# Performance work log

Hardware: AMD Instinct MI355X
Metric: run time of the kernel (lower is better)

## Reference

```python
import jax, jax.numpy as jnp
import numpy as np

N = 50000      # n_points (== n_support, non-strided)
H = 32         # neighbors per point
IN_F = 128
OUT_F = 256
MID = OUT_F // 4   # bottleneck width = 64
K = 15         # kernel points
RADIUS = 2.0
KP_EXTENT = 1.2 * RADIUS / 5.0  # config.KP_extent * radius / density_parameter
EPS = 1e-6
SLOPE = 0.1


def _wvar(k, size):
    # weight_variable: normal(scale=sqrt(2/size[-1])), zeroed outside 2*std
    std = np.sqrt(2.0 / size[-1])
    w = jax.random.normal(k, size, jnp.float32) * std
    return jnp.where(jnp.abs(w) > 2.0 * std, 0.0, w)


def setup_inputs():
    key = jax.random.key(0)
    ks = jax.random.split(key, 12)
    query_points = jax.random.uniform(ks[0], (N, 3), jnp.float32)
    support_points = query_points  # non-strided: same cloud
    neighbors_indices = jax.random.randint(ks[1], (N, H), 0, N, jnp.int32)
    features = jax.random.normal(ks[2], (N, IN_F), jnp.float32)
    kp = (jax.random.uniform(ks[3], (K, 3), jnp.float32) * 2.0 - 1.0) * (0.66 * KP_EXTENT)
    kernel_points = kp.at[0].set(0.0)  # fixed_kernel_points='center'
    w1 = _wvar(ks[4], (IN_F, MID))
    kw = _wvar(ks[5], (K, MID, MID))
    w3 = _wvar(ks[6], (MID, OUT_F))
    ws = _wvar(ks[7], (IN_F, OUT_F))
    def bnp(k, c):
        k1, k2 = jax.random.split(k)
        g = jax.random.uniform(k1, (c,), jnp.float32, 0.75, 1.25)
        b = jax.random.normal(k2, (c,), jnp.float32) * 0.1
        return g, b
    g1, b1 = bnp(ks[8], MID)
    g2, b2 = bnp(ks[9], MID)
    g3, b3 = bnp(ks[10], OUT_F)
    gs, bs = bnp(ks[11], OUT_F)
    return dict(query_points=query_points, support_points=support_points,
                neighbors_indices=neighbors_indices, features=features,
                kernel_points=kernel_points, w1=w1, g1=g1, b1=b1,
                kw=kw, g2=g2, b2=b2, w3=w3, g3=g3, b3=b3, ws=ws, gs=gs, bs=bs)


def _bn(x, g, b):
    # BatchNorm1d in training mode: batch statistics over points, biased var
    m = jnp.mean(x, 0)
    v = jnp.var(x, 0)
    return g * (x - m) * jax.lax.rsqrt(v + EPS) + b


def _lrelu(x):
    return jnp.where(x >= 0, x, SLOPE * x)


def _unary(x, w, g, b):
    return _lrelu(_bn(x @ w, g, b))


def _kpconv(q, s, inds, f, kp, kw):
    # pad support with a far shadow point and features with a zero row (faithful to KPConv)
    s_pad = jnp.concatenate([s, jnp.full((1, 3), 1e6, s.dtype)], 0)
    f_pad = jnp.concatenate([f, jnp.zeros((1, f.shape[1]), f.dtype)], 0)
    neigh = s_pad[inds]                        # [n,h,3] gather
    d = neigh - q[:, None, :]                  # [n,h,3]
    sq = jnp.sum((d[:, :, None, :] - kp[None, None, :, :]) ** 2, -1)  # [n,h,K]
    dist = jnp.sqrt(jnp.maximum(sq, 1e-12))
    infl = jnp.maximum(0.0, 1.0 - dist / KP_EXTENT)   # 'linear' KP_influence
    nf = f_pad[inds]                           # [n,h,d] gather
    wf = jnp.einsum('nhk,nhd->nkd', infl, nf)  # aggregate over neighbors
    return jnp.einsum('nkd,kdo->no', wf, kw)   # 'sum' aggregation over kernel pts


def reference(query_points, support_points, neighbors_indices, features, kernel_points,
              w1, g1, b1, kw, g2, b2, w3, g3, b3, ws, gs, bs):
    x = _unary(features, w1, g1, b1)                                     # conv1
    x = _lrelu(_bn(_kpconv(query_points, support_points, neighbors_indices,
                           x, kernel_points, kw), g2, b2))               # conv2 (KPConv)
    x = _unary(x, w3, g3, b3)                                            # conv3
    sc = _unary(features, ws, gs, bs)                                    # shortcut (non-strided)
    return _lrelu(sc + x)
```

## Files before the change

### kernel.cpp

```cpp
#include <hip/hip_runtime.h>

#define NPTS 50000
#define HN 32
#define INF1 128
#define OUTF3 256
#define MIDF 64
#define KP 15
#define EPSV 1e-6f
#define SLOPE 0.1f
#define KPE 0.48f
#define INVN (1.f / 50000.f)

typedef __attribute__((ext_vector_type(8))) short short8;
typedef __attribute__((ext_vector_type(4))) float float4v;
typedef unsigned short ushort;
typedef unsigned long long ull;

__device__ inline ushort f2bf(float f) {
    union { float f; unsigned u; } v; v.f = f;
    unsigned r = v.u + 0x7fff + ((v.u >> 16) & 1);
    return (ushort)(r >> 16);
}
__device__ inline float bf2f(ushort u) {
    union { unsigned u; float f; } v; v.u = ((unsigned)u) << 16;
    return v.f;
}


__global__ __launch_bounds__(256)
void k_repack_all(const float* __restrict__ w1, const float* __restrict__ wsw,
                  ushort* __restrict__ wpC,
                  const float* __restrict__ kw, ushort* __restrict__ wpk,
                  const float* __restrict__ w3, ushort* __restrict__ wp3) {
    int id = blockIdx.x * 256 + threadIdx.x;
    if (id < 5120) {
        int l = id & 63;
        int nt = (id >> 6) % 20, s = id / 1280;
        int n = nt * 16 + (l & 15);
        int k0 = s * 32 + ((l >> 4) & 3) * 8;
#pragma unroll
        for (int j = 0; j < 8; j++) {
            float v = (n < 64) ? w1[(k0 + j) * 64 + n] : wsw[(k0 + j) * 256 + (n - 64)];
            wpC[id * 8 + j] = f2bf(v);
        }
    } else if (id < 13312) {
        int id2 = id - 5120;
        int l2 = id2 & 63;
        int nt = (id2 >> 6) & 3, s = id2 >> 8;
        int n = nt * 16 + (l2 & 15);
        int kd0 = s * 32 + ((l2 >> 4) & 3) * 8;
#pragma unroll
        for (int j = 0; j < 8; j++) {
            int kd = kd0 + j, d = kd >> 4, kk = kd & 15;
            float v = (kk < KP) ? kw[kk * 4096 + d * 64 + n] : 0.f;
            wpk[id2 * 8 + j] = f2bf(v);
        }
    } else if (id < 15360) {
        int id3 = id - 13312;
        int l3 = id3 & 63;
        int nt = (id3 >> 6) % 16, s = id3 / 1024;
        int n = nt * 16 + (l3 & 15);
        int k0 = s * 32 + ((l3 >> 4) & 3) * 8;
#pragma unroll
        for (int j = 0; j < 8; j++)
            wp3[id3 * 8 + j] = f2bf(w3[(k0 + j) * 256 + n]);
    }
}

__global__ __launch_bounds__(256)
void k_conv1sc(const float* __restrict__ feat, const ushort* __restrict__ WpC,
               ushort* __restrict__ x1raw, ushort* __restrict__ scb,
               float* __restrict__ Sa1, float* __restrict__ Sq1,
               float* __restrict__ SaS, float* __restrict__ SqS, int M) {
    __shared__ float sred[320], qred[320];
    int t = threadIdx.x;
    int w = t >> 6, l = t & 63;
    int dl = l & 15, q4 = l >> 4;

    for (int c = t; c < 320; c += 256) { sred[c] = 0.f; qred[c] = 0.f; }
    __syncthreads();

    int m0 = blockIdx.x * 64 + w * 16;
    int row = m0 + dl;
    long arow = (row < M) ? row : (M - 1);
    const float* ap0 = feat + arow * INF1 + q4 * 8;
    short8 afr[4];
#pragma unroll
    for (int s = 0; s < 4; s++) {
        float4 a0 = *(const float4*)(ap0 + s * 32);
        float4 a1 = *(const float4*)(ap0 + s * 32 + 4);
        union { short8 v; ushort u[8]; } au;
        au.u[0] = f2bf(a0.x); au.u[1] = f2bf(a0.y); au.u[2] = f2bf(a0.z); au.u[3] = f2bf(a0.w);
        au.u[4] = f2bf(a1.x); au.u[5] = f2bf(a1.y); au.u[6] = f2bf(a1.z); au.u[7] = f2bf(a1.w);
        afr[s] = au.v;
    }
    const short8* Bp = (const short8*)WpC + l;
    int rb = q4 * 4;
#pragma unroll
    for (int half = 0; half < 2; half++) {
        float4v acc[10];
#pragma unroll
        for (int j = 0; j < 10; j++) acc[j] = (float4v){0.f, 0.f, 0.f, 0.f};
#pragma unroll
        for (int s = 0; s < 4; s++)
#pragma unroll
            for (int j = 0; j < 10; j++) {
                short8 bf = Bp[(s * 20 + half * 10 + j) * 64];
                acc[j] = __builtin_amdgcn_mfma_f32_16x16x32_bf16(afr[s], bf, acc[j], 0, 0, 0);
            }
#pragma unroll
        for (int r = 0; r < 4; r++) {
            int rr = m0 + rb + r;
            if (rr < M) {
                if (half == 0) {
                    ull pk = 0;
#pragma unroll
                    for (int j = 0; j < 4; j++)
                        pk |= ((ull)f2bf(acc[j][r])) << (16 * j);
                    *(ull*)(x1raw + (long)rr * 64 + 4 * dl) = pk;
#pragma unroll
                    for (int j = 4; j < 10; j++)
                        scb[(long)rr * 256 + (j * 16 + dl - 64)] = f2bf(acc[j][r]);
                } else {
#pragma unroll
                    for (int j = 0; j < 10; j++)
                        scb[(long)rr * 256 + ((10 + j) * 16 + dl - 64)] = f2bf(acc[j][r]);
                }
            }
        }
#pragma unroll
        for (int j = 0; j < 10; j++) {
            float s = 0.f, q = 0.f;
#pragma unroll
            for (int r = 0; r < 4; r++) {
                float v = ((m0 + rb + r) < M) ? acc[j][r] : 0.f;
                s += v; q += v * v;
            }
            s += __shfl_xor(s, 16); s += __shfl_xor(s, 32);
            q += __shfl_xor(q, 16); q += __shfl_xor(q, 32);
            if (q4 == 0) {
                atomicAdd(&sred[(half * 10 + j) * 16 + dl], s);
                atomicAdd(&qred[(half * 10 + j) * 16 + dl], q);
            }
        }
    }
    __syncthreads();
    for (int c = t; c < 320; c += 256) {
        if (c < 64) { atomicAdd(&Sa1[c], sred[c]); atomicAdd(&Sq1[c], qred[c]); }
        else        { atomicAdd(&SaS[c - 64], sred[c]); atomicAdd(&SqS[c - 64], qred[c]); }
    }
}

__global__ __launch_bounds__(256)
void k_bnx(const ushort* __restrict__ X, ushort* __restrict__ Y,
           const float* __restrict__ Sa, const float* __restrict__ Sq,
           const float* __restrict__ g, const float* __restrict__ b) {
    __shared__ float sc[64], sh[64];
    int t = threadIdx.x;
    if (t < 64) {
        float m = Sa[t] * INVN;
        float v = Sq[t] * INVN - m * m;
        float s = g[t] * rsqrtf(v + EPSV);
        sc[t] = s; sh[t] = b[t] - s * m;
    }
    __syncthreads();
    int i = blockIdx.x * 256 + t;
    long base = (long)i * 4;
    int dlp = i & 15;
    ull vin = *(const ull*)(X + base);
    ull vout = 0;
#pragma unroll
    for (int j = 0; j < 4; j++) {
        int c = j * 16 + dlp;
        float f = bf2f((ushort)((vin >> (16 * j)) & 0xffff));
        float v = f * sc[c] + sh[c];
        v = (v >= 0.f) ? v : SLOPE * v;
        vout |= ((ull)f2bf(v)) << (16 * j);
    }
    *(ull*)(Y + base) = vout;
}

__global__ __launch_bounds__(256)
void k_kpconv(const float* __restrict__ qpts, const float* __restrict__ spts,
              const int* __restrict__ nbr, const ushort* __restrict__ x1b,
              const float* __restrict__ kpp, const ushort* __restrict__ kwp,
              ushort* __restrict__ y, float* __restrict__ Sa, float* __restrict__ Sq) {
    __shared__ __align__(16) ushort wfs[16][1032];
    __shared__ float posd[4][3][HN];
    __shared__ int   sidx[4][HN];

    int t = threadIdx.x;
    int w = t >> 6, l = t & 63;
    int dl = l & 15, q4 = l >> 4;

    int kmin = (dl < KP) ? dl : (KP - 1);
    float kx = kpp[kmin * 3 + 0], ky = kpp[kmin * 3 + 1], kz = kpp[kmin * 3 + 2];

    for (int pp = 0; pp < 4; pp++) {
        int p = w * 4 + pp;
        int n = blockIdx.x * 16 + p;

        if (l < HN) {
            int idx = nbr[n * HN + l];
            sidx[w][l] = idx;
            float qx = qpts[n * 3 + 0], qy = qpts[n * 3 + 1], qz = qpts[n * 3 + 2];
            posd[w][0][l] = spts[idx * 3 + 0] - qx;
            posd[w][1][l] = spts[idx * 3 + 1] - qy;
            posd[w][2][l] = spts[idx * 3 + 2] - qz;
        }

        uint2 rj[8];
#pragma unroll
        for (int j = 0; j < 8; j++) {
            const ull* pj = (const ull*)(x1b + (long)sidx[w][q4 * 8 + j] * MIDF + 4 * dl);
            union { ull u; uint2 d; } tmp; tmp.u = *pj;
            rj[j] = tmp.d;
        }

        union { short8 v; ushort u8[8]; } afr;
#pragma unroll
        for (int j = 0; j < 8; j++) {
            int h = q4 * 8 + j;
            float ex = posd[w][0][h] - kx;
            float ey = posd[w][1][h] - ky;
            float ez = posd[w][2][h] - kz;
            float sq = ex * ex + ey * ey + ez * ez;
            float dist = sqrtf(fmaxf(sq, 1e-12f));
            float inf = fmaxf(0.f, 1.f - dist * (1.f / KPE));
            afr.u8[j] = (dl < KP) ? f2bf(inf) : (ushort)0;
        }

        union { short8 v; unsigned d[4]; } bfr[4];
#pragma unroll
        for (int dj = 0; dj < 4; dj++) {
            unsigned a_lo = rj[2 * dj].x, b_lo = rj[2 * dj + 1].x;
            unsigned a_hi = rj[2 * dj].y, b_hi = rj[2 * dj + 1].y;
            bfr[0].d[dj] = __builtin_amdgcn_perm(b_lo, a_lo, 0x05040100u);
            bfr[1].d[dj] = __builtin_amdgcn_perm(b_lo, a_lo, 0x07060302u);
            bfr[2].d[dj] = __builtin_amdgcn_perm(b_hi, a_hi, 0x05040100u);
            bfr[3].d[dj] = __builtin_amdgcn_perm(b_hi, a_hi, 0x07060302u);
        }

        float4v wfa[4];
#pragma unroll
        for (int nt = 0; nt < 4; nt++)
            wfa[nt] = __builtin_amdgcn_mfma_f32_16x16x32_bf16(
                afr.v, bfr[nt].v, (float4v){0.f, 0.f, 0.f, 0.f}, 0, 0, 0);

#pragma unroll
        for (int nt = 0; nt < 4; nt++) {
            ull pk = 0;
#pragma unroll
            for (int r = 0; r < 4; r++) {
                ushort hv = ((q4 * 4 + r) < KP) ? f2bf(wfa[nt][r]) : (ushort)0;
                pk |= ((ull)hv) << (16 * r);
            }
            *(ull*)(&wfs[p][(nt * 16 + dl) * 16 + q4 * 4]) = pk;
        }
    }
    __syncthreads();

    float4v acc = (float4v){0.f, 0.f, 0.f, 0.f};
    const ushort* arow = &wfs[dl][0] + q4 * 8;
    const short8* Bp = (const short8*)kwp + l;
#pragma unroll 8
    for (int s = 0; s < 32; s++) {
        short8 af = *(const short8*)(arow + s * 32);
        short8 bf = Bp[(s * 4 + w) * 64];
        acc = __builtin_amdgcn_mfma_f32_16x16x32_bf16(af, bf, acc, 0, 0, 0);
    }

    int o = w * 16 + dl;
    float s = 0.f, q = 0.f;
#pragma unroll
    for (int r = 0; r < 4; r++) {
        float v = acc[r];
        y[(long)(blockIdx.x * 16 + q4 * 4 + r) * MIDF + o] = f2bf(v);
        s += v; q += v * v;
    }
    s += __shfl_xor(s, 16); s += __shfl_xor(s, 32);
    q += __shfl_xor(q, 16); q += __shfl_xor(q, 32);
    if (q4 == 0) {
        atomicAdd(&Sa[o], s);
        atomicAdd(&Sq[o], q);
    }
}

__global__ __launch_bounds__(256)
void k_conv3(const ushort* __restrict__ x2raw, const ushort* __restrict__ Wp,
             ushort* __restrict__ x3b,
             const float* __restrict__ Sa2, const float* __restrict__ Sq2,
             const float* __restrict__ g2, const float* __restrict__ b2,
             float* __restrict__ Sa3, float* __restrict__ Sq3, int M) {
    __shared__ float sred[256], qred[256];
    __shared__ float scs[64], shs[64];
    int t = threadIdx.x;
    int w = t >> 6, l = t & 63;
    int dl = l & 15, q4 = l >> 4;

    if (t < 64) {
        float m = Sa2[t] * INVN;
        float v = Sq2[t] * INVN - m * m;
        float s = g2[t] * rsqrtf(v + EPSV);
        scs[t] = s; shs[t] = b2[t] - s * m;
    }
    sred[t] = 0.f; qred[t] = 0.f;
    __syncthreads();

    int m0 = blockIdx.x * 64 + w * 16;
    int row = m0 + dl;
    long arow = (row < M) ? row : (M - 1);
    const ushort* ap0 = x2raw + arow * MIDF + q4 * 8;
    short8 au2[2];
#pragma unroll
    for (int s = 0; s < 2; s++) {
        union { short8 v; ushort u[8]; } raw, cv;
        raw.v = *(const short8*)(ap0 + s * 32);
#pragma unroll
        for (int e = 0; e < 8; e++) {
            int d = s * 32 + q4 * 8 + e;
            float f = bf2f(raw.u[e]) * scs[d] + shs[d];
            f = (f >= 0.f) ? f : SLOPE * f;
            cv.u[e] = f2bf(f);
        }
        au2[s] = cv.v;
    }
    const short8* Bp = (const short8*)Wp + l;
    int rb = q4 * 4;
#pragma unroll
    for (int half = 0; half < 2; half++) {
        float4v acc[8];
#pragma unroll
        for (int j = 0; j < 8; j++) acc[j] = (float4v){0.f, 0.f, 0.f, 0.f};
#pragma unroll
        for (int s = 0; s < 2; s++)
#pragma unroll
            for (int j = 0; j < 8; j++) {
                short8 bf = Bp[(s * 16 + half * 8 + j) * 64];
                acc[j] = __builtin_amdgcn_mfma_f32_16x16x32_bf16(au2[s], bf, acc[j], 0, 0, 0);
            }
#pragma unroll
        for (int r = 0; r < 4; r++) {
            int rr = m0 + rb + r;
            if (rr < M) {
#pragma unroll
                for (int j = 0; j < 8; j++)
                    x3b[(long)rr * 256 + (half * 8 + j) * 16 + dl] = f2bf(acc[j][r]);
            }
        }
#pragma unroll
        for (int j = 0; j < 8; j++) {
            float s = 0.f, q = 0.f;
#pragma unroll
            for (int r = 0; r < 4; r++) {
                float v = ((m0 + rb + r) < M) ? acc[j][r] : 0.f;
                s += v; q += v * v;
            }
            s += __shfl_xor(s, 16); s += __shfl_xor(s, 32);
            q += __shfl_xor(q, 16); q += __shfl_xor(q, 32);
            if (q4 == 0) {
                atomicAdd(&sred[(half * 8 + j) * 16 + dl], s);
                atomicAdd(&qred[(half * 8 + j) * 16 + dl], q);
            }
        }
    }
    __syncthreads();
    atomicAdd(&Sa3[t], sred[t]);
    atomicAdd(&Sq3[t], qred[t]);
}

__global__ __launch_bounds__(256)
void k_final(const ushort* __restrict__ x3b, const ushort* __restrict__ scb,
             float* __restrict__ out,
             const float* __restrict__ a3, const float* __restrict__ q3,
             const float* __restrict__ g3, const float* __restrict__ b3,
             const float* __restrict__ aS, const float* __restrict__ qS,
             const float* __restrict__ gs, const float* __restrict__ bs) {
    __shared__ float s3[256], h3[256], sS[256], hS[256];
    int t = threadIdx.x;
    {
        float m = a3[t] * INVN;
        float v = q3[t] * INVN - m * m;
        float s = g3[t] * rsqrtf(v + EPSV);
        s3[t] = s; h3[t] = b3[t] - s * m;
        m = aS[t] * INVN;
        v = qS[t] * INVN - m * m;
        s = gs[t] * rsqrtf(v + EPSV);
        sS[t] = s; hS[t] = bs[t] - s * m;
    }
    __syncthreads();
    long i = (long)(blockIdx.x * 256 + t) * 4;
    int c0 = (int)(i & 255);
    ull va = *(const ull*)(x3b + i);
    ull vb = *(const ull*)(scb + i);
    float r[4];
#pragma unroll
    for (int j = 0; j < 4; j++) {
        int c = c0 + j;
        float x = bf2f((ushort)((va >> (16 * j)) & 0xffff)) * s3[c] + h3[c];
        x = (x >= 0.f) ? x : SLOPE * x;
        float sc = bf2f((ushort)((vb >> (16 * j)) & 0xffff)) * sS[c] + hS[c];
        sc = (sc >= 0.f) ? sc : SLOPE * sc;
        float v = x + sc;
        r[j] = (v >= 0.f) ? v : SLOPE * v;
    }
    *(float4*)(out + i) = (float4){r[0], r[1], r[2], r[3]};
}

extern "C" void kernel_launch(void* const* d_in, const int* in_sizes, int n_in,
                              void* d_out, int out_size, void* d_ws, size_t ws_size,
                              hipStream_t stream) {
    const float* qp   = (const float*)d_in[0];
    const float* sp   = (const float*)d_in[1];
    const int*   nbr  = (const int*)d_in[2];
    const float* feat = (const float*)d_in[3];
    const float* kpp  = (const float*)d_in[4];
    const float* w1   = (const float*)d_in[5];
    const float* g1   = (const float*)d_in[6];
    const float* b1   = (const float*)d_in[7];
    const float* kw   = (const float*)d_in[8];
    const float* g2   = (const float*)d_in[9];
    const float* b2   = (const float*)d_in[10];
    const float* w3   = (const float*)d_in[11];
    const float* g3   = (const float*)d_in[12];
    const float* b3   = (const float*)d_in[13];
    const float* wsw  = (const float*)d_in[14];
    const float* gs   = (const float*)d_in[15];
    const float* bs   = (const float*)d_in[16];
    float* out = (float*)d_out;

    char* base = (char*)d_ws;
    ushort* x1raw = (ushort*)(base + 0);
    ushort* x1b   = (ushort*)(base + 6400000);
    ushort* x2raw = (ushort*)(base + 12800000);
    ushort* x3b   = (ushort*)(base + 19200000);
    ushort* scb   = (ushort*)(base + 44800000);
    ushort* wpC   = (ushort*)(base + 70400000);
    ushort* wpk   = (ushort*)(base + 70481920);
    ushort* wp3   = (ushort*)(base + 70612992);
    float*  st    = (float*)(base + 70645760);
    float* acc1 = st,       *q1 = st + 64;
    float* acc2 = st + 128, *q2 = st + 192;
    float* acc3 = st + 256, *q3 = st + 512;
    float* accS = st + 768, *qS = st + 1024;

    hipMemsetAsync(st, 0, 1280 * sizeof(float), stream);

    k_repack_all<<<60, 256, 0, stream>>>(w1, wsw, wpC, kw, wpk, w3, wp3);

    k_conv1sc<<<782, 256, 0, stream>>>(feat, wpC, x1raw, scb, acc1, q1, accS, qS, NPTS);
    k_bnx<<<3125, 256, 0, stream>>>(x1raw, x1b, acc1, q1, g1, b1);

    k_kpconv<<<NPTS / 16, 256, 0, stream>>>(qp, sp, nbr, x1b, kpp, wpk, x2raw, acc2, q2);

    k_conv3<<<782, 256, 0, stream>>>(x2raw, wp3, x3b, acc2, q2, g2, b2, acc3, q3, NPTS);

    k_final<<<12500, 256, 0, stream>>>(x3b, scb, out, acc3, q3, g3, b3, accS, qS, gs, bs);
}
```

Baseline: 300.7 us.

## Pack bf16 stores in permuted layout, prefetch KPConv gathers, split MFMA accumulators

The conv1/shortcut and conv3 GEMM kernels now pack four bf16 columns into one 64-bit store using a permuted channel layout, in place of scattered 16-bit stores. The final elementwise kernel undoes this permutation when writing fp32 output, which turns its float4 stores into strided scalar stores. The KPConv kernel preloads all neighbour positions at once and double-buffers the feature gathers for the next point, so the gathered loads overlap the influence and MFMA work. Its second GEMM uses two independent accumulators to break the MFMA dependency chain. These changes cost extra registers and make the output stores less coalesced.

```diff
diff --git a/kernel.cpp b/kernel.cpp
--- a/kernel.cpp
+++ b/kernel.cpp
@@ -96,6 +96,7 @@
     }
     const short8* Bp = (const short8*)WpC + l;
     int rb = q4 * 4;
+    float sv8[4], sv9[4];
 #pragma unroll
     for (int half = 0; half < 2; half++) {
         float4v acc[10];
@@ -118,15 +119,29 @@
                     for (int j = 0; j < 4; j++)
                         pk |= ((ull)f2bf(acc[j][r])) << (16 * j);
                     *(ull*)(x1raw + (long)rr * 64 + 4 * dl) = pk;
-#pragma unroll
-                    for (int j = 4; j < 10; j++)
-                        scb[(long)rr * 256 + (j * 16 + dl - 64)] = f2bf(acc[j][r]);
+                    ull p0 = 0;
+#pragma unroll
+                    for (int e = 0; e < 4; e++)
+                        p0 |= ((ull)f2bf(acc[4 + e][r])) << (16 * e);
+                    *(ull*)(scb + (long)rr * 256 + dl * 4) = p0;
                 } else {
-#pragma unroll
-                    for (int j = 0; j < 10; j++)
-                        scb[(long)rr * 256 + ((10 + j) * 16 + dl - 64)] = f2bf(acc[j][r]);
+                    ull p1 = (ull)f2bf(sv8[r]) | ((ull)f2bf(sv9[r]) << 16)
+                           | ((ull)f2bf(acc[0][r]) << 32) | ((ull)f2bf(acc[1][r]) << 48);
+                    *(ull*)(scb + (long)rr * 256 + 64 + dl * 4) = p1;
+                    ull p2 = 0, p3 = 0;
+#pragma unroll
+                    for (int e = 0; e < 4; e++) {
+                        p2 |= ((ull)f2bf(acc[2 + e][r])) << (16 * e);
+                        p3 |= ((ull)f2bf(acc[6 + e][r])) << (16 * e);
+                    }
+                    *(ull*)(scb + (long)rr * 256 + 128 + dl * 4) = p2;
+                    *(ull*)(scb + (long)rr * 256 + 192 + dl * 4) = p3;
                 }
             }
+        }
+        if (half == 0) {
+#pragma unroll
+            for (int r = 0; r < 4; r++) { sv8[r] = acc[8][r]; sv9[r] = acc[9][r]; }
         }
 #pragma unroll
         for (int j = 0; j < 10; j++) {
@@ -186,8 +201,7 @@
               const float* __restrict__ kpp, const ushort* __restrict__ kwp,
               ushort* __restrict__ y, float* __restrict__ Sa, float* __restrict__ Sq) {
     __shared__ __align__(16) ushort wfs[16][1032];
-    __shared__ float posd[4][3][HN];
-    __shared__ int   sidx[4][HN];
+    __shared__ float posd[4][4][3][HN];
 
     int t = threadIdx.x;
     int w = t >> 6, l = t & 63;
@@ -196,34 +210,59 @@
     int kmin = (dl < KP) ? dl : (KP - 1);
     float kx = kpp[kmin * 3 + 0], ky = kpp[kmin * 3 + 1], kz = kpp[kmin * 3 + 2];
 
+    int nb = blockIdx.x * 16 + w * 4;
+
+    if (l < HN) {
+        int mi[4];
+#pragma unroll
+        for (int pp = 0; pp < 4; pp++)
+            mi[pp] = nbr[(long)(nb + pp) * HN + l];
+#pragma unroll
+        for (int pp = 0; pp < 4; pp++) {
+            float px = spts[(long)mi[pp] * 3 + 0];
+            float py = spts[(long)mi[pp] * 3 + 1];
+            float pz = spts[(long)mi[pp] * 3 + 2];
+            posd[w][pp][0][l] = px - qpts[(nb + pp) * 3 + 0];
+            posd[w][pp][1][l] = py - qpts[(nb + pp) * 3 + 1];
+            posd[w][pp][2][l] = pz - qpts[(nb + pp) * 3 + 2];
+        }
+    }
+
+    uint2 rj[2][8];
+    {
+        const int4* np = (const int4*)(nbr + (long)nb * HN + q4 * 8);
+        int4 ia = np[0], ib = np[1];
+        int id[8] = {ia.x, ia.y, ia.z, ia.w, ib.x, ib.y, ib.z, ib.w};
+#pragma unroll
+        for (int j = 0; j < 8; j++)
+            rj[0][j] = *(const uint2*)(x1b + (long)id[j] * MIDF + 4 * dl);
+    }
+
+#pragma unroll
     for (int pp = 0; pp < 4; pp++) {
-        int p = w * 4 + pp;
-        int n = blockIdx.x * 16 + p;
-
-        if (l < HN) {
-            int idx = nbr[n * HN + l];
-            sidx[w][l] = idx;
-            float qx = qpts[n * 3 + 0], qy = qpts[n * 3 + 1], qz = qpts[n * 3 + 2];
-            posd[w][0][l] = spts[idx * 3 + 0] - qx;
-            posd[w][1][l] = spts[idx * 3 + 1] - qy;
-            posd[w][2][l] = spts[idx * 3 + 2] - qz;
-        }
-
-        uint2 rj[8];
+        if (pp < 3) {
+            const int4* np = (const int4*)(nbr + (long)(nb + pp + 1) * HN + q4 * 8);
+            int4 ia = np[0], ib = np[1];
+            int id[8] = {ia.x, ia.y, ia.z, ia.w, ib.x, ib.y, ib.z, ib.w};
+#pragma unroll
+            for (int j = 0; j < 8; j++)
+                rj[(pp + 1) & 1][j] = *(const uint2*)(x1b + (long)id[j] * MIDF + 4 * dl);
+        }
+
+        union { float4 v; float f[4]; } px0, px1, py0, py1, pz0, pz1;
+        px0.v = *(const float4*)&posd[w][pp][0][q4 * 8];
+        px1.v = *(const float4*)&posd[w][pp][0][q4 * 8 + 4];
+        py0.v = *(const float4*)&posd[w][pp][1][q4 * 8];
+        py1.v = *(const float4*)&posd[w][pp][1][q4 * 8 + 4];
+        pz0.v = *(const float4*)&posd[w][pp][2][q4 * 8];
+        pz1.v = *(const float4*)&posd[w][pp][2][q4 * 8 + 4];
+
+        union { short8 v; ushort u8[8]; } afr;
 #pragma unroll
         for (int j = 0; j < 8; j++) {
-            const ull* pj = (const ull*)(x1b + (long)sidx[w][q4 * 8 + j] * MIDF + 4 * dl);
-            union { ull u; uint2 d; } tmp; tmp.u = *pj;
-            rj[j] = tmp.d;
-        }
-
-        union { short8 v; ushort u8[8]; } afr;
-#pragma unroll
-        for (int j = 0; j < 8; j++) {
-            int h = q4 * 8 + j;
-            float ex = posd[w][0][h] - kx;
-            float ey = posd[w][1][h] - ky;
-            float ez = posd[w][2][h] - kz;
+            float ex = ((j < 4) ? px0.f[j & 3] : px1.f[j & 3]) - kx;
+            float ey = ((j < 4) ? py0.f[j & 3] : py1.f[j & 3]) - ky;
+            float ez = ((j < 4) ? pz0.f[j & 3] : pz1.f[j & 3]) - kz;
             float sq = ex * ex + ey * ey + ez * ez;
             float dist = sqrtf(fmaxf(sq, 1e-12f));
             float inf = fmaxf(0.f, 1.f - dist * (1.f / KPE));
@@ -233,8 +272,8 @@
         union { short8 v; unsigned d[4]; } bfr[4];
 #pragma unroll
         for (int dj = 0; dj < 4; dj++) {
-            unsigned a_lo = rj[2 * dj].x, b_lo = rj[2 * dj + 1].x;
-            unsigned a_hi = rj[2 * dj].y, b_hi = rj[2 * dj + 1].y;
+            unsigned a_lo = rj[pp & 1][2 * dj].x, b_lo = rj[pp & 1][2 * dj + 1].x;
+            unsigned a_hi = rj[pp & 1][2 * dj].y, b_hi = rj[pp & 1][2 * dj + 1].y;
             bfr[0].d[dj] = __builtin_amdgcn_perm(b_lo, a_lo, 0x05040100u);
             bfr[1].d[dj] = __builtin_amdgcn_perm(b_lo, a_lo, 0x07060302u);
             bfr[2].d[dj] = __builtin_amdgcn_perm(b_hi, a_hi, 0x05040100u);
@@ -247,6 +286,7 @@
             wfa[nt] = __builtin_amdgcn_mfma_f32_16x16x32_bf16(
                 afr.v, bfr[nt].v, (float4v){0.f, 0.f, 0.f, 0.f}, 0, 0, 0);
 
+        int p = w * 4 + pp;
 #pragma unroll
         for (int nt = 0; nt < 4; nt++) {
             ull pk = 0;
@@ -260,15 +300,20 @@
     }
     __syncthreads();
 
-    float4v acc = (float4v){0.f, 0.f, 0.f, 0.f};
+    float4v acc0 = (float4v){0.f, 0.f, 0.f, 0.f};
+    float4v acc1 = (float4v){0.f, 0.f, 0.f, 0.f};
     const ushort* arow = &wfs[dl][0] + q4 * 8;
     const short8* Bp = (const short8*)kwp + l;
-#pragma unroll 8
-    for (int s = 0; s < 32; s++) {
-        short8 af = *(const short8*)(arow + s * 32);
-        short8 bf = Bp[(s * 4 + w) * 64];
-        acc = __builtin_amdgcn_mfma_f32_16x16x32_bf16(af, bf, acc, 0, 0, 0);
-    }
+#pragma unroll
+    for (int s = 0; s < 32; s += 2) {
+        short8 a0 = *(const short8*)(arow + s * 32);
+        short8 b0 = Bp[(s * 4 + w) * 64];
+        acc0 = __builtin_amdgcn_mfma_f32_16x16x32_bf16(a0, b0, acc0, 0, 0, 0);
+        short8 a1 = *(const short8*)(arow + (s + 1) * 32);
+        short8 b1 = Bp[((s + 1) * 4 + w) * 64];
+        acc1 = __builtin_amdgcn_mfma_f32_16x16x32_bf16(a1, b1, acc1, 0, 0, 0);
+    }
+    float4v acc = acc0 + acc1;
 
     int o = w * 16 + dl;
     float s = 0.f, q = 0.f;
@@ -344,8 +389,13 @@
             int rr = m0 + rb + r;
             if (rr < M) {
 #pragma unroll
-                for (int j = 0; j < 8; j++)
-                    x3b[(long)rr * 256 + (half * 8 + j) * 16 + dl] = f2bf(acc[j][r]);
+                for (int g = 0; g < 2; g++) {
+                    ull pk = 0;
+#pragma unroll
+                    for (int e = 0; e < 4; e++)
+                        pk |= ((ull)f2bf(acc[g * 4 + e][r])) << (16 * e);
+                    *(ull*)(x3b + (long)rr * 256 + (half * 2 + g) * 64 + dl * 4) = pk;
+                }
             }
         }
 #pragma unroll
@@ -389,22 +439,23 @@
         sS[t] = s; hS[t] = bs[t] - s * m;
     }
     __syncthreads();
-    long i = (long)(blockIdx.x * 256 + t) * 4;
-    int c0 = (int)(i & 255);
+    int ci = blockIdx.x * 256 + t;
+    long i = (long)ci * 4;
+    int li = ci & 63;
+    int cbase = ((li >> 4) << 6) + (li & 15);
+    long rowb = (long)(ci >> 6) * 256;
     ull va = *(const ull*)(x3b + i);
     ull vb = *(const ull*)(scb + i);
-    float r[4];
 #pragma unroll
     for (int j = 0; j < 4; j++) {
-        int c = c0 + j;
+        int c = cbase + j * 16;
         float x = bf2f((ushort)((va >> (16 * j)) & 0xffff)) * s3[c] + h3[c];
         x = (x >= 0.f) ? x : SLOPE * x;
         float sc = bf2f((ushort)((vb >> (16 * j)) & 0xffff)) * sS[c] + hS[c];
         sc = (sc >= 0.f) ? sc : SLOPE * sc;
         float v = x + sc;
-        r[j] = (v >= 0.f) ? v : SLOPE * v;
-    }
-    *(float4*)(out + i) = (float4){r[0], r[1], r[2], r[3]};
+        out[rowb + c] = (v >= 0.f) ? v : SLOPE * v;
+    }
 }
 
 extern "C" void kernel_launch(void* const* d_in, const int* in_sizes, int n_in,
```

Result: no change. 300.8 us (+0.0%).
